# Optimization experiments

Hardware: AMD Instinct MI355X
Metric: run time of the kernel (lower is better)

The kernel has to match this reference:

```python
import jax, jax.numpy as jnp
import numpy as np

H = 128; D = 16; L = 4
NP_ = 50000; NL_ = 10000; EPP = 500000; ELP = 100000; EPL = 100000


def _rbf(d):
    # GaussianSmearing(start=0, stop=8, num_gaussians=16)
    off = jnp.linspace(0.0, 8.0, D)
    coeff = -0.5 / ((8.0 / (D - 1)) ** 2)
    x = d[:, None] - off[None, :]
    return jnp.exp(coeff * x * x)


def _layer_norm(x, w, b, eps=1e-5):
    mu = jnp.mean(x, axis=-1, keepdims=True)
    var = jnp.var(x, axis=-1, keepdims=True)
    return (x - mu) * jax.lax.rsqrt(var + eps) * w + b


def _block(x_src, x_dst, src, dst, ea, Wf_, bf_, Ws_, bs_, bnw, bnb, lnw, lnb):
    # CGConv message: z = [x_i(dst), x_j(src), edge_attr]
    z = jnp.concatenate([x_dst[dst], x_src[src], ea], axis=-1)  # [E, 2H+D]
    m = jax.nn.sigmoid(z @ Wf_ + bf_) * jax.nn.softplus(z @ Ws_ + bs_)
    agg = jax.ops.segment_sum(m, dst, num_segments=x_dst.shape[0])
    # BatchNorm1d in eval mode with running_mean=0, running_var=1
    agg = agg * (bnw / jnp.sqrt(1.0 + 1e-5)) + bnb
    out = agg + x_dst            # CGConv internal residual
    out = _layer_norm(out, lnw, lnb)
    out = jax.nn.relu(out)
    return out + x_dst           # ResidualCGConvBlock residual (dropout=identity in eval)


def setup_inputs() -> dict:
    key = jax.random.key(0)
    ks = jax.random.split(key, 16)
    s = lambda n: 1.0 / np.sqrt(n)
    inp = {
        'x_protein': jax.random.normal(ks[0], (NP_, 6), jnp.float32),
        'x_ligand': jax.random.normal(ks[1], (NL_, 6), jnp.float32),
        'ei_pp': jnp.stack([jax.random.randint(ks[2], (EPP,), 0, NP_),
                            jax.random.randint(ks[3], (EPP,), 0, NP_)]).astype(jnp.int32),
        'ea_pp': jax.random.uniform(ks[4], (EPP,), jnp.float32, 0.0, 8.0),
        'ei_lp': jnp.stack([jax.random.randint(ks[5], (ELP,), 0, NL_),
                            jax.random.randint(ks[6], (ELP,), 0, NP_)]).astype(jnp.int32),
        'ea_lp': jax.random.uniform(ks[7], (ELP,), jnp.float32, 0.0, 8.0),
        'ei_pl': jnp.stack([jax.random.randint(ks[8], (EPL,), 0, NP_),
                            jax.random.randint(ks[9], (EPL,), 0, NL_)]).astype(jnp.int32),
        'ea_pl': jax.random.uniform(ks[10], (EPL,), jnp.float32, 0.0, 8.0),
        'Wp': jax.random.normal(ks[11], (6, H), jnp.float32) * s(6),
        'bp': jnp.zeros((H,), jnp.float32),
        'Wl': jax.random.normal(ks[12], (6, H), jnp.float32) * s(6),
        'bl': jnp.zeros((H,), jnp.float32),
        'Wf': jax.random.normal(ks[13], (L, 3, 2 * H + D, H), jnp.float32) * s(2 * H + D),
        'bf': jnp.zeros((L, 3, H), jnp.float32),
        'Ws': jax.random.normal(ks[14], (L, 3, 2 * H + D, H), jnp.float32) * s(2 * H + D),
        'bs': jnp.zeros((L, 3, H), jnp.float32),
        'bn_w': jnp.ones((L, 3, H), jnp.float32),
        'bn_b': jnp.zeros((L, 3, H), jnp.float32),
        'ln_w': jnp.ones((L, 3, H), jnp.float32),
        'ln_b': jnp.zeros((L, 3, H), jnp.float32),
        'lno_w': jnp.ones((H,), jnp.float32),
        'lno_b': jnp.zeros((H,), jnp.float32),
        'fc_w': jax.random.normal(ks[15], (H, 21), jnp.float32) * s(H),
        'fc_b': jnp.zeros((21,), jnp.float32),
    }
    return inp


def reference(x_protein, x_ligand, ei_pp, ea_pp, ei_lp, ea_lp, ei_pl, ea_pl,
              Wp, bp, Wl, bl, Wf, bf, Ws, bs, bn_w, bn_b, ln_w, ln_b,
              lno_w, lno_b, fc_w, fc_b):
    xp = x_protein @ Wp + bp
    xl = x_ligand @ Wl + bl
    rpp = _rbf(ea_pp); rlp = _rbf(ea_lp); rpl = _rbf(ea_pl)
    for l in range(L):
        # HeteroConv aggr='sum': protein receives from pp and lp; ligand from pl
        p_pp = _block(xp, xp, ei_pp[0], ei_pp[1], rpp, Wf[l, 0], bf[l, 0], Ws[l, 0], bs[l, 0],
                      bn_w[l, 0], bn_b[l, 0], ln_w[l, 0], ln_b[l, 0])
        p_lp = _block(xl, xp, ei_lp[0], ei_lp[1], rlp, Wf[l, 1], bf[l, 1], Ws[l, 1], bs[l, 1],
                      bn_w[l, 1], bn_b[l, 1], ln_w[l, 1], ln_b[l, 1])
        l_pl = _block(xp, xl, ei_pl[0], ei_pl[1], rpl, Wf[l, 2], bf[l, 2], Ws[l, 2], bs[l, 2],
                      bn_w[l, 2], bn_b[l, 2], ln_w[l, 2], ln_b[l, 2])
        xp, xl = p_pp + p_lp, l_pl
    out = _layer_norm(xp, lno_w, lno_b)
    return out @ fc_w + fc_b
```

## Files before the change

### kernel.cpp

```cpp
#include <hip/hip_runtime.h>
#include <hip/hip_bf16.h>
#include <math.h>

#define H 128
#define LOG2E 1.44269504f

typedef _Float16 f16;
typedef _Float16 f16x2 __attribute__((ext_vector_type(2)));
typedef _Float16 f16x8 __attribute__((ext_vector_type(8)));
typedef float f32x4 __attribute__((ext_vector_type(4)));
typedef float f32x2 __attribute__((ext_vector_type(2)));
typedef unsigned int uint32;

union u2h { uint32 u; f16x2 h; };
static __device__ __forceinline__ f16x2 as_h2(uint32 v){ u2h x; x.u = v; return x.h; }
static __device__ __forceinline__ uint32 pack_h2(float a, float b){
  u2h p; p.h = (f16x2){(f16)a, (f16)b}; return p.u;
}

static __device__ __forceinline__ int unperm64(int r){
  int base = r & ~63; int g = r & 63; int t = g >> 4; int j = g & 15;
  return base + 4*j + t;
}

// ... 106 lines not shown
  if (e < Epp) atomicAdd(&cpp[dpp[e]], 1);
  else if (e < Epp+Elp) atomicAdd(&clp[dlp[e-Epp]], 1);
  else if (e < Epp+Elp+Epl) atomicAdd(&cpl[dpl[e-Epp-Elp]], 1);
}

#define SCH 1024

__global__ void __launch_bounds__(256) chunksum_k(
    const int* __restrict__ counts, int NP, int NL, int Cpp, int Cpl,
    int* __restrict__ chsum){
  __shared__ int wred[4];
  int b = blockIdx.x;
  const int* cnt; int n; int ch;
  if (b < Cpp){ cnt = counts; n = NP; ch = b; }
  else if (b < 2*Cpp){ cnt = counts + NP; n = NP; ch = b - Cpp; }
  else { cnt = counts + 2*NP; n = NL; ch = b - 2*Cpp; }
  int base = ch * SCH;
  int tid = threadIdx.x;
  int s = 0;
  #pragma unroll
  for (int j=0;j<SCH/256;j++){
    int i = base + tid + j*256;
    if (i < n) s += cnt[i];
  }
  #pragma unroll
  for (int o=32;o>=1;o>>=1) s += __shfl_xor(s,o,64);
  if ((tid & 63) == 0) wred[tid>>6] = s;
  __syncthreads();
  if (tid == 0) chsum[b] = wred[0]+wred[1]+wred[2]+wred[3];
}

__global__ void __launch_bounds__(192) scanmid_k(
    int* __restrict__ chsum, int Cpp, int Cpl, int NP, int NL,
    int* __restrict__ rp_pp, int* __restrict__ rp_lp, int* __restrict__ rp_pl){
  int wid = threadIdx.x >> 6, lane = threadIdx.x & 63;
  int C, off; int* rp_end; int n;
  if (wid == 0){ C = Cpp; off = 0;      rp_end = rp_pp; n = NP; }
  else if (wid == 1){ C = Cpp; off = Cpp; rp_end = rp_lp; n = NP; }
  else { C = Cpl; off = 2*Cpp; rp_end = rp_pl; n = NL; }
  int v = (lane < C) ? chsum[off + lane] : 0;
  int x = v;
  #pragma unroll
  for (int o=1;o<64;o<<=1){
    int y = __shfl_up(x, o, 64);
    if (lane >= o) x += y;
  }
  if (lane < C) chsum[off + lane] = x - v;
  if (lane == 63) rp_end[n] = x;
}

__global__ void __launch_bounds__(1024) scanfin_k(
    const int* __restrict__ counts, int NP, int NL, int Cpp, int Cpl,
    const int* __restrict__ chsum,
    int* __restrict__ rp_pp, int* __restrict__ cur_pp,
    int* __restrict__ rp_lp, int* __restrict__ cur_lp,
    int* __restrict__ rp_pl, int* __restrict__ cur_pl){
  __shared__ int wsum[16];
  int b = blockIdx.x;
  const int* cnt; int n, ch; int* rp; int* cur;
  if (b < Cpp){ cnt = counts; n = NP; ch = b; rp = rp_pp; cur = cur_pp; }
  else if (b < 2*Cpp){ cnt = counts + NP; n = NP; ch = b - Cpp; rp = rp_lp; cur = cur_lp; }
  else { cnt = counts + 2*NP; n = NL; ch = b - 2*Cpp; rp = rp_pl; cur = cur_pl; }
  int tid = threadIdx.x, lane = tid & 63, wid = tid >> 6;
  int i = ch*SCH + tid;
  int v = (i < n) ? cnt[i] : 0;
  int x = v;
  #pragma unroll
  for (int o=1;o<64;o<<=1){
    int y = __shfl_up(x, o, 64);
    if (lane >= o) x += y;
  }
  if (lane == 63) wsum[wid] = x;
  __syncthreads();
  if (wid == 0 && lane < 16){
    int w = wsum[lane];
    #pragma unroll
    for (int o=1;o<16;o<<=1){
      int y = __shfl_up(w, o, 64);
      if (lane >= o) w += y;
    }
    wsum[lane] = w;
  }
  __syncthreads();
  int waveoff = (wid == 0) ? 0 : wsum[wid-1];
  int ex = chsum[b] + waveoff + x - v;
  if (i < n){ rp[i] = ex; cur[i] = ex; }
}

__global__ void fill3_k(const int* __restrict__ ei_pp, const float* __restrict__ ea_pp, int Epp,
                        const int* __restrict__ ei_lp, const float* __restrict__ ea_lp, int Elp,
                        const int* __restrict__ ei_pl, const float* __restrict__ ea_pl, int Epl,
                        int* __restrict__ cur_pp, int2* __restrict__ e2_pp,
                        int* __restrict__ cur_lp, int2* __restrict__ e2_lp,
                        int* __restrict__ cur_pl, int2* __restrict__ e2_pl){
  int e = blockIdx.x*blockDim.x + threadIdx.x;
  if (e < Epp){
    int p = atomicAdd(&cur_pp[ei_pp[Epp + e]], 1);
    e2_pp[p] = make_int2(ei_pp[e], __float_as_int(ea_pp[e]));
  } else if (e < Epp+Elp){
    int i = e - Epp;
    int p = atomicAdd(&cur_lp[ei_lp[Elp + i]], 1);
    e2_lp[p] = make_int2(ei_lp[i], __float_as_int(ea_lp[i]));
  } else if (e < Epp+Elp+Epl){
    int i = e - Epp - Elp;
    int p = atomicAdd(&cur_pl[ei_pl[Epl + i]], 1);
    e2_pl[p] = make_int2(ei_pl[i], __float_as_int(ea_pl[i]));
  }
}

__global__ void __launch_bounds__(256) degbin_hist(
    const int* __restrict__ rp_pp, const int* __restrict__ rp_lp,
    const int* __restrict__ rp_pl, int NP, int NL, int* __restrict__ hist){
  __shared__ int lh[128];
  int t = threadIdx.x;
  if (t < 128) lh[t] = 0;
  __syncthreads();
  int i = blockIdx.x*256 + t;
  if (i < NP){
    int d = (rp_pp[i+1]-rp_pp[i]) + (rp_lp[i+1]-rp_lp[i]);
    if (d > 63) d = 63;
    atomicAdd(&lh[63 - d], 1);
  } else if (i < NP+NL){
    int n = i - NP;
    int d = rp_pl[n+1]-rp_pl[n];
    if (d > 63) d = 63;
    atomicAdd(&lh[64 + 63 - d], 1);
  }
  __syncthreads();
  if (t < 128 && lh[t]) atomicAdd(&hist[t], lh[t]);
}

__global__ void __launch_bounds__(128) degbin_scan(
    const int* __restrict__ hist, int* __restrict__ cursor){
  int t = threadIdx.x, lane = t & 63;
  int v = hist[t];
  int x = v;
  #pragma unroll
  for (int o=1;o<64;o<<=1){
    int y = __shfl_up(x, o, 64);
    if (lane >= o) x += y;
  }
  cursor[t] = x - v;
}

__global__ void __launch_bounds__(256) degbin_scatter(
    const int* __restrict__ rp_pp, const int* __restrict__ rp_lp,
    const int* __restrict__ rp_pl, int NP, int NL,
    int* __restrict__ cursor, int* __restrict__ perm){
  __shared__ int lh[128], lbase[128], lrank[128];
  int t = threadIdx.x;
  if (t < 128){ lh[t] = 0; lrank[t] = 0; }
  __syncthreads();
  int i = blockIdx.x*256 + t;
  int bin = -1, n = 0;
  if (i < NP){
    n = i;
    int d = (rp_pp[i+1]-rp_pp[i]) + (rp_lp[i+1]-rp_lp[i]);
    if (d > 63) d = 63;
    bin = 63 - d;
  } else if (i < NP+NL){
    n = i - NP;
    int d = rp_pl[n+1]-rp_pl[n];
    if (d > 63) d = 63;
    bin = 64 + 63 - d;
  }
  if (bin >= 0) atomicAdd(&lh[bin], 1);
  __syncthreads();
  if (t < 128 && lh[t]) lbase[t] = atomicAdd(&cursor[t], lh[t]);
  __syncthreads();
  if (bin >= 0){
    int r = atomicAdd(&lrank[bin], 1);
    perm[(bin < 64 ? 0 : NP) + lbase[bin] + r] = n;
  }
}

#define GR 8
__global__ void __launch_bounds__(256) gemm_tables(
    const f16* __restrict__ Xp, const f16* __restrict__ Wtp,
    const float* __restrict__ Biasp, f16* __restrict__ Outp,
    int strips_p, int chunks_p, int pblocks,
    const f16* __restrict__ Xl, const f16* __restrict__ Wtl,
    const float* __restrict__ Biasl, f16* __restrict__ Outl,
    int strips_l, int chunks_l){
  int b = blockIdx.x;
  int w = threadIdx.x >> 6;
  const f16 *X, *Wt; const float* Bias; f16* Out; int N, strips, g, chunk;
  if (b < pblocks){
    int c = (b >> 5)*8 + (b & 7);
    if (c >= chunks_p) return;
    X=Xp; Wt=Wtp; Bias=Biasp; Out=Outp; N=1024; strips=strips_p;
    g = ((b >> 3) & 3)*4 + w; chunk = c;
  } else {
    int bl = b - pblocks;
    int c = (bl >> 4)*8 + (bl & 7);
    if (c >= chunks_l) return;
    X=Xl; Wt=Wtl; Bias=Biasl; Out=Outl; N=512; strips=strips_l;
    g = ((bl >> 3) & 1)*4 + w; chunk = c;
  }
  int n0 = g << 6;
  int lane = threadIdx.x & 63;
  int lr = lane & 15, lq = lane >> 4;
  const f16x8* B0 = (const f16x8*)(const void*)(Wt + (size_t)(n0      + lr)*H);
  const f16x8* B1 = (const f16x8*)(const void*)(Wt + (size_t)(n0 + 16 + lr)*H);
  const f16x8* B2 = (const f16x8*)(const void*)(Wt + (size_t)(n0 + 32 + lr)*H);
  const f16x8* B3 = (const f16x8*)(const void*)(Wt + (size_t)(n0 + 48 + lr)*H);
  f16x8 b0_0=B0[lq], b0_1=B0[4+lq], b0_2=B0[8+lq], b0_3=B0[12+lq];
  f16x8 b1_0=B1[lq], b1_1=B1[4+lq], b1_2=B1[8+lq], b1_3=B1[12+lq];
  f16x8 b2_0=B2[lq], b2_1=B2[4+lq], b2_2=B2[8+lq], b2_3=B2[12+lq];
  f16x8 b3_0=B3[lq], b3_1=B3[4+lq], b3_2=B3[8+lq], b3_3=B3[12+lq];
  float4 bias = ((const float4*)(const void*)(Bias + n0))[lr];
  #pragma unroll 2
  for (int r=0;r<GR;r++){
    int strip = chunk*GR + r;
    if (strip >= strips) break;
    int m0 = strip << 4;
    const f16x8* A = (const f16x8*)(const void*)(X + (size_t)(m0+lr)*H);
    f16x8 a0 = A[lq], a1 = A[4+lq], a2 = A[8+lq], a3 = A[12+lq];
    f32x4 acc0 = {0.f,0.f,0.f,0.f}, acc1 = acc0, acc2 = acc0, acc3 = acc0;
    acc0 = __builtin_amdgcn_mfma_f32_16x16x32_f16(a0, b0_0, acc0, 0, 0, 0);
    acc1 = __builtin_amdgcn_mfma_f32_16x16x32_f16(a0, b1_0, acc1, 0, 0, 0);
    acc2 = __builtin_amdgcn_mfma_f32_16x16x32_f16(a0, b2_0, acc2, 0, 0, 0);
    acc3 = __builtin_amdgcn_mfma_f32_16x16x32_f16(a0, b3_0, acc3, 0, 0, 0);
    acc0 = __builtin_amdgcn_mfma_f32_16x16x32_f16(a1, b0_1, acc0, 0, 0, 0);
    acc1 = __builtin_amdgcn_mfma_f32_16x16x32_f16(a1, b1_1, acc1, 0, 0, 0);
    acc2 = __builtin_amdgcn_mfma_f32_16x16x32_f16(a1, b2_1, acc2, 0, 0, 0);
    acc3 = __builtin_amdgcn_mfma_f32_16x16x32_f16(a1, b3_1, acc3, 0, 0, 0);
    acc0 = __builtin_amdgcn_mfma_f32_16x16x32_f16(a2, b0_2, acc0, 0, 0, 0);
    acc1 = __builtin_amdgcn_mfma_f32_16x16x32_f16(a2, b1_2, acc1, 0, 0, 0);
    acc2 = __builtin_amdgcn_mfma_f32_16x16x32_f16(a2, b2_2, acc2, 0, 0, 0);
    acc3 = __builtin_amdgcn_mfma_f32_16x16x32_f16(a2, b3_2, acc3, 0, 0, 0);
    acc0 = __builtin_amdgcn_mfma_f32_16x16x32_f16(a3, b0_3, acc0, 0, 0, 0);
    acc1 = __builtin_amdgcn_mfma_f32_16x16x32_f16(a3, b1_3, acc1, 0, 0, 0);
    acc2 = __builtin_amdgcn_mfma_f32_16x16x32_f16(a3, b2_3, acc2, 0, 0, 0);
    acc3 = __builtin_amdgcn_mfma_f32_16x16x32_f16(a3, b3_3, acc3, 0, 0, 0);
    #pragma unroll
    for (int rr=0;rr<4;rr++){
      int row = m0 + lq*4 + rr;
      uint2 pk;
      pk.x = pack_h2(acc0[rr] + bias.x, acc1[rr] + bias.y);
      pk.y = pack_h2(acc2[rr] + bias.z, acc3[rr] + bias.w);
      *(uint2*)(void*)(Out + (size_t)row*N + n0 + 4*lr) = pk;
    }
  }
}

static __device__ __forceinline__ float act_msg(float F, float S){
  float sig = __builtin_amdgcn_rcpf(1.f + __builtin_amdgcn_exp2f(-F));
  float e   = __builtin_amdgcn_exp2f(fminf(S, 86.f));
  return sig * __builtin_amdgcn_logf(1.f + e);
}

#define BN_SCL (0.9999950000374997f * 0.69314718f)

static __device__ __forceinline__ void edge_nb(uint2 g, uint2 t,
                                               f16x2 fd2, f16x2 sd2, f32x2& acc){
  f16x2 F = (as_h2(g.x) + as_h2(t.x)) + fd2;
  f16x2 S = (as_h2(g.y) + as_h2(t.y)) + sd2;
  acc.x += act_msg((float)F.x, (float)S.x);
  acc.y += act_msg((float)F.y, (float)S.y);
}

static __device__ __forceinline__ void ln_stats_w(float v0, float v1, float& mu, float& var){
  float s = v0 + v1, q = v0*v0 + v1*v1;
  #pragma unroll
  for (int o=32;o>=1;o>>=1){ s += __shfl_xor(s,o,64); q += __shfl_xor(q,o,64); }
  mu = s * (1.f/128.f);
  var = q * (1.f/128.f) - mu*mu;
}

static __device__ __forceinline__ void aggregate(
    const int2* __restrict__ ev_arr, int e0, int e1,
    const uint2* __restrict__ G, int gstride, int goff,
    const uint2* __restrict__ Tb, int lane,
    f16x2 fd2, f16x2 sd2, f32x2& acc)
{
  for (int base = e0; base < e1; base += 64){
    int idx = base + lane;
    int2 ev = ev_arr[(idx < e1) ? idx : (e1-1)];
    float dd = __int_as_float(ev.y);
    int bnv = (int)__fmaf_rn(dd, (float)NBIN/8.0f, 0.5f);
    bnv = (bnv > NBIN) ? NBIN : bnv;
    int cnt = e1 - base; cnt = (cnt > 64) ? 64 : cnt;
    uint2 gA, tA, gB, tB, gC, tC;
    #define LDJ(gX, tX, j) { \
      int s_ = __builtin_amdgcn_readlane(ev.x, (j)); \
      int b_ = __builtin_amdgcn_readlane(bnv, (j)); \
      gX = G[(size_t)s_*gstride + goff + lane]; \
      tX = Tb[(size_t)b_*64 + lane]; }
    LDJ(gA, tA, 0);
    if (cnt > 1) LDJ(gB, tB, 1);
    if (cnt > 2) LDJ(gC, tC, 2);
    int j = 0;
    for (; j+5 < cnt; j += 3){
      edge_nb(gA, tA, fd2, sd2, acc); LDJ(gA, tA, j+3);
      edge_nb(gB, tB, fd2, sd2, acc); LDJ(gB, tB, j+4);
      edge_nb(gC, tC, fd2, sd2, acc); LDJ(gC, tC, j+5);
    }
    int rem = cnt - j;
    edge_nb(gA, tA, fd2, sd2, acc);
    if (rem > 3) LDJ(gA, tA, j+3);
    if (rem > 1) edge_nb(gB, tB, fd2, sd2, acc);
    if (rem > 4) LDJ(gB, tB, j+4);
    if (rem > 2) edge_nb(gC, tC, fd2, sd2, acc);
    if (rem > 3) edge_nb(gA, tA, fd2, sd2, acc);
    if (rem > 4) edge_nb(gB, tB, fd2, sd2, acc);
    #undef LDJ
  }
}

static __device__ __forceinline__ void rel_post(
    f32x2 acc, float2 bwf, float2 bb, float2 lw, float2 lb,
    float xx, float xy, float& o0, float& o1)
{
  float v0 = acc.x * bwf.x + bb.x + xx;
  float v1 = acc.y * bwf.y + bb.y + xy;
  float mu, var; ln_stats_w(v0, v1, mu, var);
  float rs = rsqrtf(var + 1e-5f);
  o0 = fmaxf((v0-mu)*rs*lw.x + lb.x, 0.f) + xx;
  o1 = fmaxf((v1-mu)*rs*lw.y + lb.y, 0.f) + xy;
}

__global__ void __launch_bounds__(128) node_update(
    const f16* __restrict__ PT, const f16* __restrict__ LT,
    const f16* __restrict__ xp, const f16* __restrict__ xl,
    const int* __restrict__ pp_rp, const int2* __restrict__ pp_e2,
    const int* __restrict__ lp_rp, const int2* __restrict__ lp_e2,
    const int* __restrict__ pl_rp, const int2* __restrict__ pl_e2,
    const f16* __restrict__ T2,
    const float* __restrict__ bn_w, const float* __restrict__ bn_b,
    const float* __restrict__ ln_w, const float* __restrict__ ln_b,
    const int* __restrict__ perm,
    f16* __restrict__ xp_o, f16* __restrict__ xl_o,
    int layer, int NP, int NL, int PB)
{
  int wave = threadIdx.x >> 6;
  int lane = threadIdx.x & 63;
  const uint2* PTg = (const uint2*)(const void*)PT;
  if ((int)blockIdx.x < PB){
    int idx0 = blockIdx.x*4 + wave*2;
    if (idx0 >= NP) return;
    const uint32* PTu = (const uint32*)(const void*)PT;
    const uint2*  LTg = (const uint2*)(const void*)LT;
    const uint32* Xu  = (const uint32*)(const void*)xp;
    uint32* Xo = (uint32*)(void*)xp_o;
    int pr0 = layer*3, pr1 = layer*3 + 1;
    const uint2* Tb0 = (const uint2*)(const void*)(T2 + (size_t)pr0*(NBIN+1)*256);
    const uint2* Tb1 = (const uint2*)(const void*)(T2 + (size_t)pr1*(NBIN+1)*256);
    float2 bw0 = ((const float2*)(const void*)(bn_w + pr0*H))[lane];
    float2 bb0 = ((const float2*)(const void*)(bn_b + pr0*H))[lane];
    float2 lw0 = ((const float2*)(const void*)(ln_w + pr0*H))[lane];
    float2 lb0 = ((const float2*)(const void*)(ln_b + pr0*H))[lane];
    float2 bw1 = ((const float2*)(const void*)(bn_w + pr1*H))[lane];
    float2 bb1 = ((const float2*)(const void*)(bn_b + pr1*H))[lane];
    float2 lw1 = ((const float2*)(const void*)(ln_w + pr1*H))[lane];
    float2 lb1 = ((const float2*)(const void*)(ln_b + pr1*H))[lane];
    bw0.x *= BN_SCL; bw0.y *= BN_SCL; bw1.x *= BN_SCL; bw1.y *= BN_SCL;
    int nodeA = perm[idx0];
    bool hasB = (idx0 + 1 < NP);
    int nodeB = perm[hasB ? (idx0 + 1) : idx0];
    int a_pp0 = pp_rp[nodeA], a_pp1 = pp_rp[nodeA+1];
    int a_lp0 = lp_rp[nodeA], a_lp1 = lp_rp[nodeA+1];
    int b_pp0 = pp_rp[nodeB], b_pp1 = pp_rp[nodeB+1];
    int b_lp0 = lp_rp[nodeB], b_lp1 = lp_rp[nodeB+1];
    uint32 xBu  = Xu[(size_t)nodeB*64 + lane];
    uint32 fdB0 = PTu[(size_t)nodeB*512 + 256 + lane];
    uint32 sdB0 = PTu[(size_t)nodeB*512 + 320 + lane];
    uint32 fdB1 = PTu[(size_t)nodeB*512 + 384 + lane];
    uint32 sdB1 = PTu[(size_t)nodeB*512 + 448 + lane];
    uint32 xAu  = Xu[(size_t)nodeA*64 + lane];
    uint32 fdA0 = PTu[(size_t)nodeA*512 + 256 + lane];
    uint32 sdA0 = PTu[(size_t)nodeA*512 + 320 + lane];
    uint32 fdA1 = PTu[(size_t)nodeA*512 + 384 + lane];
    uint32 sdA1 = PTu[(size_t)nodeA*512 + 448 + lane];
    {
      f16x2 xh = as_h2(xAu);
      float xx = (float)xh.x, xy = (float)xh.y;
      f32x2 acc0 = {0.f,0.f}, acc1 = {0.f,0.f};
      aggregate(pp_e2, a_pp0, a_pp1, PTg, 256, 0, Tb0, lane, as_h2(fdA0), as_h2(sdA0), acc0);
      aggregate(lp_e2, a_lp0, a_lp1, LTg, 128, 0, Tb1, lane, as_h2(fdA1), as_h2(sdA1), acc1);
      float o1_0, o1_1, o2_0, o2_1;
      rel_post(acc0, bw0, bb0, lw0, lb0, xx, xy, o1_0, o1_1);
      rel_post(acc1, bw1, bb1, lw1, lb1, xx, xy, o2_0, o2_1);
      Xo[(size_t)nodeA*64 + lane] = pack_h2(o1_0 + o2_0, o1_1 + o2_1);
    }
    if (hasB){
      f16x2 xh = as_h2(xBu);
      float xx = (float)xh.x, xy = (float)xh.y;
      f32x2 acc0 = {0.f,0.f}, acc1 = {0.f,0.f};
      aggregate(pp_e2, b_pp0, b_pp1, PTg, 256, 0, Tb0, lane, as_h2(fdB0), as_h2(sdB0), acc0);
      aggregate(lp_e2, b_lp0, b_lp1, LTg, 128, 0, Tb1, lane, as_h2(fdB1), as_h2(sdB1), acc1);
      float o1_0, o1_1, o2_0, o2_1;
      rel_post(acc0, bw0, bb0, lw0, lb0, xx, xy, o1_0, o1_1);
      rel_post(acc1, bw1, bb1, lw1, lb1, xx, xy, o2_0, o2_1);
      Xo[(size_t)nodeB*64 + lane] = pack_h2(o1_0 + o2_0, o1_1 + o2_1);
    }
  } else {
    int idx0 = (blockIdx.x - PB)*4 + wave*2;
    if (idx0 >= NL) return;
    const uint32* LTu = (const uint32*)(const void*)LT;
    const uint32* Xu  = (const uint32*)(const void*)xl;
    uint32* Xo = (uint32*)(void*)xl_o;
    int pr2 = layer*3 + 2;
    const uint2* Tb2 = (const uint2*)(const void*)(T2 + (size_t)pr2*(NBIN+1)*256);
    float2 bw2 = ((const float2*)(const void*)(bn_w + pr2*H))[lane];
    float2 bb2 = ((const float2*)(const void*)(bn_b + pr2*H))[lane];
    float2 lw2 = ((const float2*)(const void*)(ln_w + pr2*H))[lane];
    float2 lb2 = ((const float2*)(const void*)(ln_b + pr2*H))[lane];
    bw2.x *= BN_SCL; bw2.y *= BN_SCL;
    int nodeA = perm[NP + idx0];
    bool hasB = (idx0 + 1 < NL);
    int nodeB = perm[NP + (hasB ? (idx0 + 1) : idx0)];
    int a_e0 = pl_rp[nodeA], a_e1 = pl_rp[nodeA+1];
    int b_e0 = pl_rp[nodeB], b_e1 = pl_rp[nodeB+1];
    uint32 xBu  = Xu[(size_t)nodeB*64 + lane];
    uint32 fdB2 = LTu[(size_t)nodeB*256 + 128 + lane];
    uint32 sdB2 = LTu[(size_t)nodeB*256 + 192 + lane];
    uint32 xAu  = Xu[(size_t)nodeA*64 + lane];
    uint32 fdA2 = LTu[(size_t)nodeA*256 + 128 + lane];
    uint32 sdA2 = LTu[(size_t)nodeA*256 + 192 + lane];
    {
      f16x2 xh = as_h2(xAu);
      float xx = (float)xh.x, xy = (float)xh.y;
      f32x2 acc = {0.f,0.f};
      aggregate(pl_e2, a_e0, a_e1, PTg, 256, 64, Tb2, lane, as_h2(fdA2), as_h2(sdA2), acc);
      float o0, o1;
      rel_post(acc, bw2, bb2, lw2, lb2, xx, xy, o0, o1);
      Xo[(size_t)nodeA*64 + lane] = pack_h2(o0, o1);
    }
    if (hasB){
      f16x2 xh = as_h2(xBu);
      float xx = (float)xh.x, xy = (float)xh.y;
      f32x2 acc = {0.f,0.f};
      aggregate(pl_e2, b_e0, b_e1, PTg, 256, 64, Tb2, lane, as_h2(fdB2), as_h2(sdB2), acc);
      float o0, o1;
      rel_post(acc, bw2, bb2, lw2, lb2, xx, xy, o0, o1);
      Xo[(size_t)nodeB*64 + lane] = pack_h2(o0, o1);
    }
  }
}

__global__ void __launch_bounds__(256) final_k(const f16* __restrict__ xp,
    const float* __restrict__ lnw, const float* __restrict__ lnb,
    const f16* __restrict__ fwhi, const f16* __restrict__ fwlo,
    const float* __restrict__ fcb, float* __restrict__ out, int N){
  int wave = threadIdx.x >> 6, lane = threadIdx.x & 63;
  int m0 = (blockIdx.x*4 + wave) << 4;
  if (m0 >= N) return;
  int lr = lane & 15, lq = lane >> 4;
  int node = m0 + lr; if (node >= N) node = N - 1;
  const f16x8* X = (const f16x8*)(const void*)(xp + (size_t)node*H);
  f16x8 x0 = X[lq], x1 = X[4+lq], x2 = X[8+lq], x3 = X[12+lq];
  float s = 0.f, q = 0.f;
  #pragma unroll
  for (int i=0;i<8;i++){
    float a=(float)x0[i], b=(float)x1[i], c=(float)x2[i], d=(float)x3[i];
    s += a+b+c+d; q += a*a+b*b+c*c+d*d;
  }
  s += __shfl_xor(s,16,64); q += __shfl_xor(q,16,64);
  s += __shfl_xor(s,32,64); q += __shfl_xor(q,32,64);
  float mu = s*(1.f/128.f), var = q*(1.f/128.f) - mu*mu;
  float rs = rsqrtf(var + 1e-5f);
  f16x8 xs0 = x0, xs1 = x1, xs2 = x2, xs3 = x3;
  f16x8 ah[4], al[4];
  const float4* LW = (const float4*)(const void*)lnw;
  const float4* LB = (const float4*)(const void*)lnb;
  #define MKFRAG(F, XS) { \
    int b4 = F*8 + lq*2; \
    float4 w0 = LW[b4], w1 = LW[b4+1]; \
    float4 c0 = LB[b4], c1 = LB[b4+1]; \
    float l0=((float)XS[0]-mu)*rs*w0.x + c0.x; \
    float l1=((float)XS[1]-mu)*rs*w0.y + c0.y; \
    float l2=((float)XS[2]-mu)*rs*w0.z + c0.z; \
    float l3=((float)XS[3]-mu)*rs*w0.w + c0.w; \
    float l4=((float)XS[4]-mu)*rs*w1.x + c1.x; \
    float l5=((float)XS[5]-mu)*rs*w1.y + c1.y; \
    float l6=((float)XS[6]-mu)*rs*w1.z + c1.z; \
    float l7=((float)XS[7]-mu)*rs*w1.w + c1.w; \
    f16x8 hh = {(f16)l0,(f16)l1,(f16)l2,(f16)l3,(f16)l4,(f16)l5,(f16)l6,(f16)l7}; \
    f16x8 ll = {(f16)(l0-(float)hh[0]),(f16)(l1-(float)hh[1]), \
                (f16)(l2-(float)hh[2]),(f16)(l3-(float)hh[3]), \
                (f16)(l4-(float)hh[4]),(f16)(l5-(float)hh[5]), \
                (f16)(l6-(float)hh[6]),(f16)(l7-(float)hh[7])}; \
    ah[F] = hh; al[F] = ll; }
  MKFRAG(0, xs0); MKFRAG(1, xs1); MKFRAG(2, xs2); MKFRAG(3, xs3);
  #undef MKFRAG
  const f16x8* BH0 = (const f16x8*)(const void*)(fwhi + (size_t)lr*128);
  const f16x8* BH1 = (const f16x8*)(const void*)(fwhi + (size_t)(16+lr)*128);
  const f16x8* BL0 = (const f16x8*)(const void*)(fwlo + (size_t)lr*128);
  const f16x8* BL1 = (const f16x8*)(const void*)(fwlo + (size_t)(16+lr)*128);
  f32x4 acc0 = {0.f,0.f,0.f,0.f}, acc1 = acc0;
// ... 11 lines not shown
  float bias0 = fcb[lr];
  float bias1 = (lr < 5) ? fcb[16 + lr] : 0.f;
  #pragma unroll
  for (int rr=0; rr<4; rr++){
    int row = m0 + lq*4 + rr;
    if (row < N){
      out[(size_t)row*21 + lr] = acc0[rr] + bias0;
      if (lr < 5) out[(size_t)row*21 + 16 + lr] = acc1[rr] + bias1;
    }
  }
}

extern "C" void kernel_launch(void* const* d_in, const int* in_sizes, int n_in,
                              void* d_out, int out_size, void* d_ws, size_t ws_size,
                              hipStream_t stream){
  const float* x_protein = (const float*)d_in[0];
  const float* x_ligand  = (const float*)d_in[1];
  const int*   ei_pp = (const int*)d_in[2];
  const float* ea_pp = (const float*)d_in[3];
  const int*   ei_lp = (const int*)d_in[4];
  const float* ea_lp = (const float*)d_in[5];
  const int*   ei_pl = (const int*)d_in[6];
  const float* ea_pl = (const float*)d_in[7];
  const float* Wp  = (const float*)d_in[8];
  const float* bp  = (const float*)d_in[9];
  const float* Wl  = (const float*)d_in[10];
  const float* bl  = (const float*)d_in[11];
  const float* Wf  = (const float*)d_in[12];
  const float* bfv = (const float*)d_in[13];
  const float* Wsv = (const float*)d_in[14];
  const float* bsv = (const float*)d_in[15];
  const float* bn_w = (const float*)d_in[16];
  const float* bn_b = (const float*)d_in[17];
  const float* ln_w = (const float*)d_in[18];
  const float* ln_b = (const float*)d_in[19];
  const float* lno_w = (const float*)d_in[20];
  const float* lno_b = (const float*)d_in[21];
  const float* fc_w = (const float*)d_in[22];
  const float* fc_b = (const float*)d_in[23];

  int NP  = in_sizes[0]/6, NL = in_sizes[1]/6;
  int EPP = in_sizes[3], ELP = in_sizes[5], EPL = in_sizes[7];

  char* ws = (char*)d_ws;
  size_t off = 0;
  auto alloc = [&](size_t bytes)->void*{
    void* p = ws + off; off = (off + bytes + 255) & ~(size_t)255; return p;
  };

  f16* xpA = (f16*)alloc((size_t)NP*H*2);
  f16* xpB = (f16*)alloc((size_t)NP*H*2);
  f16* xlA = (f16*)alloc((size_t)NL*H*2);
  f16* xlB = (f16*)alloc((size_t)NL*H*2);
  f16* PT    = (f16*)alloc((size_t)NP*1024*2);
  f16* LT    = (f16*)alloc((size_t)NL*512*2);
  f16* Wt_p  = (f16*)alloc((size_t)4*1024*H*2);
  f16* Wt_l  = (f16*)alloc((size_t)4*512*H*2);
  float* Bias_p = (float*)alloc((size_t)4*1024*4);
  float* Bias_l = (float*)alloc((size_t)4*512*4);
  f16* T2    = (f16*)alloc((size_t)12*(NBIN+1)*256*2);
  f16* fwhi  = (f16*)alloc((size_t)32*128*2);
  f16* fwlo  = (f16*)alloc((size_t)32*128*2);
  int* counts = (int*)alloc((size_t)(2*NP+NL)*4);
  int* rp_pp  = (int*)alloc((size_t)(NP+1)*4);
  int* cur_pp = (int*)alloc((size_t)NP*4);
  int* rp_lp  = (int*)alloc((size_t)(NP+1)*4);
  int* cur_lp = (int*)alloc((size_t)NP*4);
  int* rp_pl  = (int*)alloc((size_t)(NL+1)*4);
  int* cur_pl = (int*)alloc((size_t)NL*4);
  int2* e2_pp = (int2*)alloc((size_t)EPP*8);
  int2* e2_lp = (int2*)alloc((size_t)ELP*8);
  int2* e2_pl = (int2*)alloc((size_t)EPL*8);
  int Cpp = (NP + SCH - 1) / SCH;
  int Cpl = (NL + SCH - 1) / SCH;
  int* chsum = (int*)alloc((size_t)(2*Cpp + Cpl)*4);
  int* dhist  = (int*)alloc(128*4);
  int* dcur   = (int*)alloc(128*4);
  int* perm   = (int*)alloc((size_t)(NP+NL)*4);
  (void)ws_size; (void)n_in; (void)out_size;

  size_t prep_total = (size_t)PREP_WP_N + PREP_WL_N + RBF_N + FC_N + (size_t)(NP+NL)*H;
  prep_all<<<(prep_total+255)/256, 256, 0, stream>>>(Wf, Wsv, bfv, bsv,
      Wt_p, Bias_p, Wt_l, Bias_l, T2,
      fc_w, fwhi, fwlo,
      x_protein, Wp, bp, xpA, NP,
      x_ligand,  Wl, bl, xlA, NL);
  hipMemsetAsync(counts, 0, (size_t)(2*NP+NL)*4, stream);
  hipMemsetAsync(dhist, 0, 128*4, stream);
  int* cnt_pp = counts; int* cnt_lp = counts + NP; int* cnt_pl = counts + 2*NP;
  int Etot = EPP + ELP + EPL;
  hist3_k<<<(Etot+255)/256, 256, 0, stream>>>(ei_pp+EPP, EPP, ei_lp+ELP, ELP, ei_pl+EPL, EPL,
                                              cnt_pp, cnt_lp, cnt_pl);
  chunksum_k<<<2*Cpp + Cpl, 256, 0, stream>>>(counts, NP, NL, Cpp, Cpl, chsum);
  scanmid_k<<<1, 192, 0, stream>>>(chsum, Cpp, Cpl, NP, NL, rp_pp, rp_lp, rp_pl);
  scanfin_k<<<2*Cpp + Cpl, 1024, 0, stream>>>(counts, NP, NL, Cpp, Cpl, chsum,
                                              rp_pp, cur_pp, rp_lp, cur_lp, rp_pl, cur_pl);
  fill3_k<<<(Etot+255)/256, 256, 0, stream>>>(ei_pp, ea_pp, EPP, ei_lp, ea_lp, ELP,
                                              ei_pl, ea_pl, EPL,
                                              cur_pp, e2_pp, cur_lp, e2_lp, cur_pl, e2_pl);
  int nbks = (NP + NL + 255) / 256;
  degbin_hist<<<nbks, 256, 0, stream>>>(rp_pp, rp_lp, rp_pl, NP, NL, dhist);
  degbin_scan<<<1, 128, 0, stream>>>(dhist, dcur);
  degbin_scatter<<<nbks, 256, 0, stream>>>(rp_pp, rp_lp, rp_pl, NP, NL, dcur, perm);

  f16* xp_cur = xpA; f16* xp_nxt = xpB;
  f16* xl_cur = xlA; f16* xl_nxt = xlB;
  int strips_p = NP >> 4, strips_l = NL >> 4;
  int chunks_p = (strips_p + GR - 1) / GR;
  int chunks_l = (strips_l + GR - 1) / GR;
  int pblocks = ((chunks_p + 7) / 8) * 32;
  int lblocks = ((chunks_l + 7) / 8) * 16;
  int PB = (NP + 3) / 4, LB = (NL + 3) / 4;
  for (int l=0; l<4; l++){
    gemm_tables<<<pblocks + lblocks, 256, 0, stream>>>(
        xp_cur, Wt_p + (size_t)l*1024*H, Bias_p + l*1024, PT, strips_p, chunks_p, pblocks,
        xl_cur, Wt_l + (size_t)l*512*H,  Bias_l + l*512,  LT, strips_l, chunks_l);
    node_update<<<PB + LB, 128, 0, stream>>>(PT, LT, xp_cur, xl_cur,
        rp_pp, e2_pp, rp_lp, e2_lp, rp_pl, e2_pl, T2,
        bn_w, bn_b, ln_w, ln_b, perm, xp_nxt, xl_nxt, l, NP, NL, PB);
    f16* t;
    t = xp_cur; xp_cur = xp_nxt; xp_nxt = t;
    t = xl_cur; xl_cur = xl_nxt; xl_nxt = t;
  }

  int fstrips = (NP + 15) >> 4;
  final_k<<<(fstrips+3)/4, 256, 0, stream>>>(xp_cur, lno_w, lno_b,
      fwhi, fwlo, fc_b, (float*)d_out, NP);
}
```

Baseline: 679.4 us.

## Merge pp and lp edge lists and precompute gather offsets and RBF bins

Protein-side pp and lp edges now go into one concatenated CSR segment per node. Each edge entry stores a precomputed element offset into a unified PT/LT table buffer and a global RBF bin index, so the per-layer aggregation no longer computes bins or strides. Node_update now processes one node per wave over a single merged edge loop with a per-edge branch selecting the relation accumulator, instead of two nodes per wave with separate loops. This removes per-layer bin arithmetic and loop overhead, at the cost of a per-edge branch and halved per-wave node work.

```diff
diff --git a/kernel.cpp b/kernel.cpp
--- a/kernel.cpp
+++ b/kernel.cpp
@@ -182,14 +182,14 @@
 __global__ void __launch_bounds__(1024) scanfin_k(
     const int* __restrict__ counts, int NP, int NL, int Cpp, int Cpl,
     const int* __restrict__ chsum,
-    int* __restrict__ rp_pp, int* __restrict__ cur_pp,
-    int* __restrict__ rp_lp, int* __restrict__ cur_lp,
+    int* __restrict__ rp_pp,
+    int* __restrict__ rp_lp,
     int* __restrict__ rp_pl, int* __restrict__ cur_pl){
   __shared__ int wsum[16];
   int b = blockIdx.x;
   const int* cnt; int n, ch; int* rp; int* cur;
-  if (b < Cpp){ cnt = counts; n = NP; ch = b; rp = rp_pp; cur = cur_pp; }
-  else if (b < 2*Cpp){ cnt = counts + NP; n = NP; ch = b - Cpp; rp = rp_lp; cur = cur_lp; }
+  if (b < Cpp){ cnt = counts; n = NP; ch = b; rp = rp_pp; cur = 0; }
+  else if (b < 2*Cpp){ cnt = counts + NP; n = NP; ch = b - Cpp; rp = rp_lp; cur = 0; }
   else { cnt = counts + 2*NP; n = NL; ch = b - 2*Cpp; rp = rp_pl; cur = cur_pl; }
   int tid = threadIdx.x, lane = tid & 63, wid = tid >> 6;
   int i = ch*SCH + tid;
@@ -214,40 +214,24 @@
   __syncthreads();
   int waveoff = (wid == 0) ? 0 : wsum[wid-1];
   int ex = chsum[b] + waveoff + x - v;
-  if (i < n){ rp[i] = ex; cur[i] = ex; }
-}
-
-__global__ void fill3_k(const int* __restrict__ ei_pp, const float* __restrict__ ea_pp, int Epp,
-                        const int* __restrict__ ei_lp, const float* __restrict__ ea_lp, int Elp,
-                        const int* __restrict__ ei_pl, const float* __restrict__ ea_pl, int Epl,
-                        int* __restrict__ cur_pp, int2* __restrict__ e2_pp,
-                        int* __restrict__ cur_lp, int2* __restrict__ e2_lp,
-                        int* __restrict__ cur_pl, int2* __restrict__ e2_pl){
-  int e = blockIdx.x*blockDim.x + threadIdx.x;
-  if (e < Epp){
-    int p = atomicAdd(&cur_pp[ei_pp[Epp + e]], 1);
-    e2_pp[p] = make_int2(ei_pp[e], __float_as_int(ea_pp[e]));
-  } else if (e < Epp+Elp){
-    int i = e - Epp;
-    int p = atomicAdd(&cur_lp[ei_lp[Elp + i]], 1);
-    e2_lp[p] = make_int2(ei_lp[i], __float_as_int(ea_lp[i]));
-  } else if (e < Epp+Elp+Epl){
-    int i = e - Epp - Elp;
-    int p = atomicAdd(&cur_pl[ei_pl[Epl + i]], 1);
-    e2_pl[p] = make_int2(ei_pl[i], __float_as_int(ea_pl[i]));
-  }
+  if (i < n){ rp[i] = ex; if (cur) cur[i] = ex; }
 }
 
 __global__ void __launch_bounds__(256) degbin_hist(
     const int* __restrict__ rp_pp, const int* __restrict__ rp_lp,
-    const int* __restrict__ rp_pl, int NP, int NL, int* __restrict__ hist){
+    const int* __restrict__ rp_pl, int NP, int NL, int* __restrict__ hist,
+    int* __restrict__ cur_pp, int* __restrict__ cur_lp){
   __shared__ int lh[128];
   int t = threadIdx.x;
   if (t < 128) lh[t] = 0;
   __syncthreads();
   int i = blockIdx.x*256 + t;
   if (i < NP){
-    int d = (rp_pp[i+1]-rp_pp[i]) + (rp_lp[i+1]-rp_lp[i]);
+    int a0 = rp_pp[i], a1 = rp_pp[i+1];
+    int b0 = rp_lp[i], b1 = rp_lp[i+1];
+    cur_pp[i] = a0 + b0;
+    cur_lp[i] = a1 + b0;
+    int d = (a1-a0) + (b1-b0);
     if (d > 63) d = 63;
     atomicAdd(&lh[63 - d], 1);
   } else if (i < NP+NL){
@@ -301,6 +285,37 @@
   if (bin >= 0){
     int r = atomicAdd(&lrank[bin], 1);
     perm[(bin < 64 ? 0 : NP) + lbase[bin] + r] = n;
+  }
+}
+
+__global__ void fill3_k(const int* __restrict__ ei_pp, const float* __restrict__ ea_pp, int Epp,
+                        const int* __restrict__ ei_lp, const float* __restrict__ ea_lp, int Elp,
+                        const int* __restrict__ ei_pl, const float* __restrict__ ea_pl, int Epl,
+                        int* __restrict__ cur_pp, int* __restrict__ cur_lp,
+                        int2* __restrict__ epc,
+                        int* __restrict__ cur_pl, int2* __restrict__ elc,
+                        int LT_OFF){
+  int e = blockIdx.x*blockDim.x + threadIdx.x;
+  if (e < Epp){
+    int src = ei_pp[e]; float d = ea_pp[e];
+    int bin = (int)__fmaf_rn(d, (float)NBIN/8.0f, 0.5f);
+    bin = (bin > NBIN) ? NBIN : bin;
+    int p = atomicAdd(&cur_pp[ei_pp[Epp + e]], 1);
+    epc[p] = make_int2(src*256, bin);
+  } else if (e < Epp+Elp){
+    int i = e - Epp;
+    int src = ei_lp[i]; float d = ea_lp[i];
+    int bin = (int)__fmaf_rn(d, (float)NBIN/8.0f, 0.5f);
+    bin = (bin > NBIN) ? NBIN : bin;
+    int p = atomicAdd(&cur_lp[ei_lp[Elp + i]], 1);
+    epc[p] = make_int2(LT_OFF + src*128, (NBIN+1) + bin);
+  } else if (e < Epp+Elp+Epl){
+    int i = e - Epp - Elp;
+    int src = ei_pl[i]; float d = ea_pl[i];
+    int bin = (int)__fmaf_rn(d, (float)NBIN/8.0f, 0.5f);
+    bin = (bin > NBIN) ? NBIN : bin;
+    int p = atomicAdd(&cur_pl[ei_pl[Epl + i]], 1);
+    elc[p] = make_int2(src*256 + 64, 2*(NBIN+1) + bin);
   }
 }
 
@@ -398,42 +413,79 @@
   var = q * (1.f/128.f) - mu*mu;
 }
 
-static __device__ __forceinline__ void aggregate(
+static __device__ __forceinline__ void aggregate_m(
+    const int2* __restrict__ ev_arr, int e0, int es, int e1,
+    const uint2* __restrict__ G, const uint2* __restrict__ Tb, int lane,
+    f16x2 fdA, f16x2 sdA, f16x2 fdB, f16x2 sdB,
+    f32x2& accA, f32x2& accB)
+{
+  for (int base = e0; base < e1; base += 64){
+    int idx = base + lane;
+    int2 ev = ev_arr[(idx < e1) ? idx : (e1-1)];
+    int cnt = e1 - base; cnt = (cnt > 64) ? 64 : cnt;
+    uint2 g0,t0,g1,t1,g2,t2;
+    #define LDJ(gX, tX, j) { \
+      int go = __builtin_amdgcn_readlane(ev.x, (j)); \
+      int tb = __builtin_amdgcn_readlane(ev.y, (j)); \
+      gX = G[(size_t)go + lane]; \
+      tX = Tb[(size_t)tb*64 + lane]; }
+    #define EDG(gX, tX, j) { \
+      if (base + (j) < es) edge_nb(gX, tX, fdA, sdA, accA); \
+      else                 edge_nb(gX, tX, fdB, sdB, accB); }
+    LDJ(g0,t0,0);
+    if (cnt > 1) LDJ(g1,t1,1);
+    if (cnt > 2) LDJ(g2,t2,2);
+    int j = 0;
+    for (; j+5 < cnt; j += 3){
+      EDG(g0,t0,j);   LDJ(g0,t0,j+3);
+      EDG(g1,t1,j+1); LDJ(g1,t1,j+4);
+      EDG(g2,t2,j+2); LDJ(g2,t2,j+5);
+    }
+    int rem = cnt - j;
+    EDG(g0,t0,j);
+    if (rem > 3) LDJ(g0,t0,j+3);
+    if (rem > 1) EDG(g1,t1,j+1);
+    if (rem > 4) LDJ(g1,t1,j+4);
+    if (rem > 2) EDG(g2,t2,j+2);
+    if (rem > 3) EDG(g0,t0,j+3);
+    if (rem > 4) EDG(g1,t1,j+4);
+    #undef LDJ
+    #undef EDG
+  }
+}
+
+static __device__ __forceinline__ void aggregate_s(
     const int2* __restrict__ ev_arr, int e0, int e1,
-    const uint2* __restrict__ G, int gstride, int goff,
-    const uint2* __restrict__ Tb, int lane,
+    const uint2* __restrict__ G, const uint2* __restrict__ Tb, int lane,
     f16x2 fd2, f16x2 sd2, f32x2& acc)
 {
   for (int base = e0; base < e1; base += 64){
     int idx = base + lane;
     int2 ev = ev_arr[(idx < e1) ? idx : (e1-1)];
-    float dd = __int_as_float(ev.y);
-    int bnv = (int)__fmaf_rn(dd, (float)NBIN/8.0f, 0.5f);
-    bnv = (bnv > NBIN) ? NBIN : bnv;
     int cnt = e1 - base; cnt = (cnt > 64) ? 64 : cnt;
-    uint2 gA, tA, gB, tB, gC, tC;
+    uint2 g0,t0,g1,t1,g2,t2;
     #define LDJ(gX, tX, j) { \
-      int s_ = __builtin_amdgcn_readlane(ev.x, (j)); \
-      int b_ = __builtin_amdgcn_readlane(bnv, (j)); \
-      gX = G[(size_t)s_*gstride + goff + lane]; \
-      tX = Tb[(size_t)b_*64 + lane]; }
-    LDJ(gA, tA, 0);
-    if (cnt > 1) LDJ(gB, tB, 1);
-    if (cnt > 2) LDJ(gC, tC, 2);
+      int go = __builtin_amdgcn_readlane(ev.x, (j)); \
+      int tb = __builtin_amdgcn_readlane(ev.y, (j)); \
+      gX = G[(size_t)go + lane]; \
+      tX = Tb[(size_t)tb*64 + lane]; }
+    LDJ(g0,t0,0);
+    if (cnt > 1) LDJ(g1,t1,1);
+    if (cnt > 2) LDJ(g2,t2,2);
     int j = 0;
     for (; j+5 < cnt; j += 3){
-      edge_nb(gA, tA, fd2, sd2, acc); LDJ(gA, tA, j+3);
-      edge_nb(gB, tB, fd2, sd2, acc); LDJ(gB, tB, j+4);
-      edge_nb(gC, tC, fd2, sd2, acc); LDJ(gC, tC, j+5);
+      edge_nb(g0,t0,fd2,sd2,acc); LDJ(g0,t0,j+3);
+      edge_nb(g1,t1,fd2,sd2,acc); LDJ(g1,t1,j+4);
+      edge_nb(g2,t2,fd2,sd2,acc); LDJ(g2,t2,j+5);
     }
     int rem = cnt - j;
-    edge_nb(gA, tA, fd2, sd2, acc);
-    if (rem > 3) LDJ(gA, tA, j+3);
-    if (rem > 1) edge_nb(gB, tB, fd2, sd2, acc);
-    if (rem > 4) LDJ(gB, tB, j+4);
-    if (rem > 2) edge_nb(gC, tC, fd2, sd2, acc);
-    if (rem > 3) edge_nb(gA, tA, fd2, sd2, acc);
-    if (rem > 4) edge_nb(gB, tB, fd2, sd2, acc);
+    edge_nb(g0,t0,fd2,sd2,acc);
+    if (rem > 3) LDJ(g0,t0,j+3);
+    if (rem > 1) edge_nb(g1,t1,fd2,sd2,acc);
+    if (rem > 4) LDJ(g1,t1,j+4);
+    if (rem > 2) edge_nb(g2,t2,fd2,sd2,acc);
+    if (rem > 3) edge_nb(g0,t0,fd2,sd2,acc);
+    if (rem > 4) edge_nb(g1,t1,fd2,sd2,acc);
     #undef LDJ
   }
 }
@@ -451,11 +503,11 @@
 }
 
 __global__ void __launch_bounds__(128) node_update(
-    const f16* __restrict__ PT, const f16* __restrict__ LT,
+    const f16* __restrict__ PT,
     const f16* __restrict__ xp, const f16* __restrict__ xl,
-    const int* __restrict__ pp_rp, const int2* __restrict__ pp_e2,
-    const int* __restrict__ lp_rp, const int2* __restrict__ lp_e2,
-    const int* __restrict__ pl_rp, const int2* __restrict__ pl_e2,
+    const int* __restrict__ pp_rp, const int* __restrict__ lp_rp,
+    const int* __restrict__ pl_rp,
+    const int2* __restrict__ epc, const int2* __restrict__ elc,
     const f16* __restrict__ T2,
     const float* __restrict__ bn_w, const float* __restrict__ bn_b,
     const float* __restrict__ ln_w, const float* __restrict__ ln_b,
@@ -466,106 +518,66 @@
   int wave = threadIdx.x >> 6;
   int lane = threadIdx.x & 63;
   const uint2* PTg = (const uint2*)(const void*)PT;
+  const uint2* TbL = ((const uint2*)(const void*)T2) + (size_t)layer*3*(NBIN+1)*64;
   if ((int)blockIdx.x < PB){
-    int idx0 = blockIdx.x*4 + wave*2;
-    if (idx0 >= NP) return;
+    int idx = blockIdx.x*2 + wave;
+    if (idx >= NP) return;
+    int node = perm[idx];
     const uint32* PTu = (const uint32*)(const void*)PT;
-    const uint2*  LTg = (const uint2*)(const void*)LT;
     const uint32* Xu  = (const uint32*)(const void*)xp;
-    uint32* Xo = (uint32*)(void*)xp_o;
+    int a0 = pp_rp[node], a1 = pp_rp[node+1];
+    int b0 = lp_rp[node], b1 = lp_rp[node+1];
+    int e0 = __builtin_amdgcn_readfirstlane(a0 + b0);
+    int es = __builtin_amdgcn_readfirstlane(a1 + b0);
+    int e1 = __builtin_amdgcn_readfirstlane(a1 + b1);
+    uint32 xu  = Xu[(size_t)node*64 + lane];
+    f16x2 fd0 = as_h2(PTu[(size_t)node*512 + 256 + lane]);
+    f16x2 sd0 = as_h2(PTu[(size_t)node*512 + 320 + lane]);
+    f16x2 fd1 = as_h2(PTu[(size_t)node*512 + 384 + lane]);
+    f16x2 sd1 = as_h2(PTu[(size_t)node*512 + 448 + lane]);
+    f32x2 acc0 = {0.f,0.f}, acc1 = {0.f,0.f};
+    aggregate_m(epc, e0, es, e1, PTg, TbL, lane, fd0, sd0, fd1, sd1, acc0, acc1);
+    f16x2 xh = as_h2(xu);
+    float xx = (float)xh.x, xy = (float)xh.y;
     int pr0 = layer*3, pr1 = layer*3 + 1;
-    const uint2* Tb0 = (const uint2*)(const void*)(T2 + (size_t)pr0*(NBIN+1)*256);
-    const uint2* Tb1 = (const uint2*)(const void*)(T2 + (size_t)pr1*(NBIN+1)*256);
     float2 bw0 = ((const float2*)(const void*)(bn_w + pr0*H))[lane];
     float2 bb0 = ((const float2*)(const void*)(bn_b + pr0*H))[lane];
     float2 lw0 = ((const float2*)(const void*)(ln_w + pr0*H))[lane];
     float2 lb0 = ((const float2*)(const void*)(ln_b + pr0*H))[lane];
+    bw0.x *= BN_SCL; bw0.y *= BN_SCL;
+    float o1_0, o1_1, o2_0, o2_1;
+    rel_post(acc0, bw0, bb0, lw0, lb0, xx, xy, o1_0, o1_1);
     float2 bw1 = ((const float2*)(const void*)(bn_w + pr1*H))[lane];
     float2 bb1 = ((const float2*)(const void*)(bn_b + pr1*H))[lane];
     float2 lw1 = ((const float2*)(const void*)(ln_w + pr1*H))[lane];
     float2 lb1 = ((const float2*)(const void*)(ln_b + pr1*H))[lane];
-    bw0.x *= BN_SCL; bw0.y *= BN_SCL; bw1.x *= BN_SCL; bw1.y *= BN_SCL;
-    int nodeA = perm[idx0];
-    bool hasB = (idx0 + 1 < NP);
-    int nodeB = perm[hasB ? (idx0 + 1) : idx0];
-    int a_pp0 = pp_rp[nodeA], a_pp1 = pp_rp[nodeA+1];
-    int a_lp0 = lp_rp[nodeA], a_lp1 = lp_rp[nodeA+1];
-    int b_pp0 = pp_rp[nodeB], b_pp1 = pp_rp[nodeB+1];
-    int b_lp0 = lp_rp[nodeB], b_lp1 = lp_rp[nodeB+1];
-    uint32 xBu  = Xu[(size_t)nodeB*64 + lane];
-    uint32 fdB0 = PTu[(size_t)nodeB*512 + 256 + lane];
-    uint32 sdB0 = PTu[(size_t)nodeB*512 + 320 + lane];
-    uint32 fdB1 = PTu[(size_t)nodeB*512 + 384 + lane];
-    uint32 sdB1 = PTu[(size_t)nodeB*512 + 448 + lane];
-    uint32 xAu  = Xu[(size_t)nodeA*64 + lane];
-    uint32 fdA0 = PTu[(size_t)nodeA*512 + 256 + lane];
-    uint32 sdA0 = PTu[(size_t)nodeA*512 + 320 + lane];
-    uint32 fdA1 = PTu[(size_t)nodeA*512 + 384 + lane];
-    uint32 sdA1 = PTu[(size_t)nodeA*512 + 448 + lane];
-    {
-      f16x2 xh = as_h2(xAu);
-      float xx = (float)xh.x, xy = (float)xh.y;
-      f32x2 acc0 = {0.f,0.f}, acc1 = {0.f,0.f};
-      aggregate(pp_e2, a_pp0, a_pp1, PTg, 256, 0, Tb0, lane, as_h2(fdA0), as_h2(sdA0), acc0);
-      aggregate(lp_e2, a_lp0, a_lp1, LTg, 128, 0, Tb1, lane, as_h2(fdA1), as_h2(sdA1), acc1);
-      float o1_0, o1_1, o2_0, o2_1;
-      rel_post(acc0, bw0, bb0, lw0, lb0, xx, xy, o1_0, o1_1);
-      rel_post(acc1, bw1, bb1, lw1, lb1, xx, xy, o2_0, o2_1);
-      Xo[(size_t)nodeA*64 + lane] = pack_h2(o1_0 + o2_0, o1_1 + o2_1);
-    }
-    if (hasB){
-      f16x2 xh = as_h2(xBu);
-      float xx = (float)xh.x, xy = (float)xh.y;
-      f32x2 acc0 = {0.f,0.f}, acc1 = {0.f,0.f};
-      aggregate(pp_e2, b_pp0, b_pp1, PTg, 256, 0, Tb0, lane, as_h2(fdB0), as_h2(sdB0), acc0);
-      aggregate(lp_e2, b_lp0, b_lp1, LTg, 128, 0, Tb1, lane, as_h2(fdB1), as_h2(sdB1), acc1);
-      float o1_0, o1_1, o2_0, o2_1;
-      rel_post(acc0, bw0, bb0, lw0, lb0, xx, xy, o1_0, o1_1);
-      rel_post(acc1, bw1, bb1, lw1, lb1, xx, xy, o2_0, o2_1);
-      Xo[(size_t)nodeB*64 + lane] = pack_h2(o1_0 + o2_0, o1_1 + o2_1);
-    }
+    bw1.x *= BN_SCL; bw1.y *= BN_SCL;
+    rel_post(acc1, bw1, bb1, lw1, lb1, xx, xy, o2_0, o2_1);
+    ((uint32*)(void*)xp_o)[(size_t)node*64 + lane] = pack_h2(o1_0 + o2_0, o1_1 + o2_1);
   } else {
-    int idx0 = (blockIdx.x - PB)*4 + wave*2;
-    if (idx0 >= NL) return;
-    const uint32* LTu = (const uint32*)(const void*)LT;
+    int idx = (blockIdx.x - PB)*2 + wave;
+    if (idx >= NL) return;
+    int node = perm[NP + idx];
+    const uint32* LTu = (const uint32*)(const void*)(PT + (size_t)NP*1024);
     const uint32* Xu  = (const uint32*)(const void*)xl;
-    uint32* Xo = (uint32*)(void*)xl_o;
+    int e0 = __builtin_amdgcn_readfirstlane(pl_rp[node]);
+    int e1 = __builtin_amdgcn_readfirstlane(pl_rp[node+1]);
+    uint32 xu  = Xu[(size_t)node*64 + lane];
+    f16x2 fd2 = as_h2(LTu[(size_t)node*256 + 128 + lane]);
+    f16x2 sd2 = as_h2(LTu[(size_t)node*256 + 192 + lane]);
+    f32x2 acc = {0.f,0.f};
+    aggregate_s(elc, e0, e1, PTg, TbL, lane, fd2, sd2, acc);
+    f16x2 xh = as_h2(xu);
+    float xx = (float)xh.x, xy = (float)xh.y;
     int pr2 = layer*3 + 2;
-    const uint2* Tb2 = (const uint2*)(const void*)(T2 + (size_t)pr2*(NBIN+1)*256);
     float2 bw2 = ((const float2*)(const void*)(bn_w + pr2*H))[lane];
     float2 bb2 = ((const float2*)(const void*)(bn_b + pr2*H))[lane];
     float2 lw2 = ((const float2*)(const void*)(ln_w + pr2*H))[lane];
     float2 lb2 = ((const float2*)(const void*)(ln_b + pr2*H))[lane];
     bw2.x *= BN_SCL; bw2.y *= BN_SCL;
-    int nodeA = perm[NP + idx0];
-    bool hasB = (idx0 + 1 < NL);
-    int nodeB = perm[NP + (hasB ? (idx0 + 1) : idx0)];
-    int a_e0 = pl_rp[nodeA], a_e1 = pl_rp[nodeA+1];
-    int b_e0 = pl_rp[nodeB], b_e1 = pl_rp[nodeB+1];
-    uint32 xBu  = Xu[(size_t)nodeB*64 + lane];
-    uint32 fdB2 = LTu[(size_t)nodeB*256 + 128 + lane];
-    uint32 sdB2 = LTu[(size_t)nodeB*256 + 192 + lane];
-    uint32 xAu  = Xu[(size_t)nodeA*64 + lane];
-    uint32 fdA2 = LTu[(size_t)nodeA*256 + 128 + lane];
-    uint32 sdA2 = LTu[(size_t)nodeA*256 + 192 + lane];
-    {
-      f16x2 xh = as_h2(xAu);
-      float xx = (float)xh.x, xy = (float)xh.y;
-      f32x2 acc = {0.f,0.f};
-      aggregate(pl_e2, a_e0, a_e1, PTg, 256, 64, Tb2, lane, as_h2(fdA2), as_h2(sdA2), acc);
-      float o0, o1;
-      rel_post(acc, bw2, bb2, lw2, lb2, xx, xy, o0, o1);
-      Xo[(size_t)nodeA*64 + lane] = pack_h2(o0, o1);
-    }
-    if (hasB){
-      f16x2 xh = as_h2(xBu);
-      float xx = (float)xh.x, xy = (float)xh.y;
-      f32x2 acc = {0.f,0.f};
-      aggregate(pl_e2, b_e0, b_e1, PTg, 256, 64, Tb2, lane, as_h2(fdB2), as_h2(sdB2), acc);
-      float o0, o1;
-      rel_post(acc, bw2, bb2, lw2, lb2, xx, xy, o0, o1);
-      Xo[(size_t)nodeB*64 + lane] = pack_h2(o0, o1);
-    }
+    float o0, o1;
+    rel_post(acc, bw2, bb2, lw2, lb2, xx, xy, o0, o1);
+    ((uint32*)(void*)xl_o)[(size_t)node*64 + lane] = pack_h2(o0, o1);
   }
 }
 
@@ -683,8 +695,8 @@
   f16* xpB = (f16*)alloc((size_t)NP*H*2);
   f16* xlA = (f16*)alloc((size_t)NL*H*2);
   f16* xlB = (f16*)alloc((size_t)NL*H*2);
-  f16* PT    = (f16*)alloc((size_t)NP*1024*2);
-  f16* LT    = (f16*)alloc((size_t)NL*512*2);
+  f16* PT    = (f16*)alloc(((size_t)NP*1024 + (size_t)NL*512)*2);
+  f16* LT    = PT + (size_t)NP*1024;
   f16* Wt_p  = (f16*)alloc((size_t)4*1024*H*2);
   f16* Wt_l  = (f16*)alloc((size_t)4*512*H*2);
   float* Bias_p = (float*)alloc((size_t)4*1024*4);
@@ -699,9 +711,8 @@
   int* cur_lp = (int*)alloc((size_t)NP*4);
   int* rp_pl  = (int*)alloc((size_t)(NL+1)*4);
   int* cur_pl = (int*)alloc((size_t)NL*4);
-  int2* e2_pp = (int2*)alloc((size_t)EPP*8);
-  int2* e2_lp = (int2*)alloc((size_t)ELP*8);
-  int2* e2_pl = (int2*)alloc((size_t)EPL*8);
+  int2* epc   = (int2*)alloc((size_t)(EPP+ELP)*8);
+  int2* elc   = (int2*)alloc((size_t)EPL*8);
   int Cpp = (NP + SCH - 1) / SCH;
   int Cpl = (NL + SCH - 1) / SCH;
   int* chsum = (int*)alloc((size_t)(2*Cpp + Cpl)*4);
@@ -725,12 +736,13 @@
   chunksum_k<<<2*Cpp + Cpl, 256, 0, stream>>>(counts, NP, NL, Cpp, Cpl, chsum);
   scanmid_k<<<1, 192, 0, stream>>>(chsum, Cpp, Cpl, NP, NL, rp_pp, rp_lp, rp_pl);
   scanfin_k<<<2*Cpp + Cpl, 1024, 0, stream>>>(counts, NP, NL, Cpp, Cpl, chsum,
-                                              rp_pp, cur_pp, rp_lp, cur_lp, rp_pl, cur_pl);
+                                              rp_pp, rp_lp, rp_pl, cur_pl);
+  int nbks = (NP + NL + 255) / 256;
+  degbin_hist<<<nbks, 256, 0, stream>>>(rp_pp, rp_lp, rp_pl, NP, NL, dhist,
+                                        cur_pp, cur_lp);
   fill3_k<<<(Etot+255)/256, 256, 0, stream>>>(ei_pp, ea_pp, EPP, ei_lp, ea_lp, ELP,
                                               ei_pl, ea_pl, EPL,
-                                              cur_pp, e2_pp, cur_lp, e2_lp, cur_pl, e2_pl);
-  int nbks = (NP + NL + 255) / 256;
-  degbin_hist<<<nbks, 256, 0, stream>>>(rp_pp, rp_lp, rp_pl, NP, NL, dhist);
+                                              cur_pp, cur_lp, epc, cur_pl, elc, NP*256);
   degbin_scan<<<1, 128, 0, stream>>>(dhist, dcur);
   degbin_scatter<<<nbks, 256, 0, stream>>>(rp_pp, rp_lp, rp_pl, NP, NL, dcur, perm);
 
@@ -741,13 +753,13 @@
   int chunks_l = (strips_l + GR - 1) / GR;
   int pblocks = ((chunks_p + 7) / 8) * 32;
   int lblocks = ((chunks_l + 7) / 8) * 16;
-  int PB = (NP + 3) / 4, LB = (NL + 3) / 4;
+  int PB = (NP + 1) / 2, LB = (NL + 1) / 2;
   for (int l=0; l<4; l++){
     gemm_tables<<<pblocks + lblocks, 256, 0, stream>>>(
         xp_cur, Wt_p + (size_t)l*1024*H, Bias_p + l*1024, PT, strips_p, chunks_p, pblocks,
         xl_cur, Wt_l + (size_t)l*512*H,  Bias_l + l*512,  LT, strips_l, chunks_l);
-    node_update<<<PB + LB, 128, 0, stream>>>(PT, LT, xp_cur, xl_cur,
-        rp_pp, e2_pp, rp_lp, e2_lp, rp_pl, e2_pl, T2,
+    node_update<<<PB + LB, 128, 0, stream>>>(PT, xp_cur, xl_cur,
+        rp_pp, rp_lp, rp_pl, epc, elc, T2,
         bn_w, bn_b, ln_w, ln_b, perm, xp_nxt, xl_nxt, l, NP, NL, PB);
     f16* t;
     t = xp_cur; xp_cur = xp_nxt; xp_nxt = t;
```

New measurement: 684.6 us. No clear change (+0.8%).
